# Kernel tuning notes

Hardware: AMD Instinct MI355X
Metric: run time of the kernel (lower is better)

## Reference

```python
import jax, jax.numpy as jnp
import numpy as np

HID = 5120       # hidden_size
H = 32           # num_heads (TP shard)
Q_RANK = 1536    # q_lora_rank
KV_RANK = 512    # kv_lora_rank
D_NOPE = 128     # qk_nope_head_dim
D_ROPE = 64      # qk_rope_head_dim
DV = 128         # v_head_dim
Q_HEAD = D_NOPE + D_ROPE
T = 2048
EPS = 1e-6
ROPE_BASE = 10000.0
SCALE = Q_HEAD ** -0.5
NEG = jnp.finfo(jnp.float32).min


def rmsnorm(x, w):
    return x * jax.lax.rsqrt(jnp.mean(x * x, axis=-1, keepdims=True) + EPS) * w


def rope(x, pos):
    # half-split (GPT-NeoX style) rotary; the torch module permutes weights in
    # _update_pe so that interleaved RoPE becomes exactly this half-split form.
    half = x.shape[-1] // 2
    inv = 1.0 / (ROPE_BASE ** (jnp.arange(half, dtype=jnp.float32) / half))
    ang = pos.astype(jnp.float32)[:, None] * inv          # [T, half]
    cos, sin = jnp.cos(ang), jnp.sin(ang)
    if x.ndim == 3:                                       # [T, H, D]
        cos, sin = cos[:, None, :], sin[:, None, :]
    x1, x2 = jnp.split(x, 2, axis=-1)
    return jnp.concatenate([x1 * cos - x2 * sin, x2 * cos + x1 * sin], axis=-1)


def setup_inputs() -> dict:
    key = jax.random.key(0)
    ks = jax.random.split(key, 10)
    s = 0.02
    return {
        'hidden_states': jax.random.normal(ks[0], (1, T, HID), jnp.float32),
        'position_ids': jnp.arange(T, dtype=jnp.int64),
        'w_q_a': jax.random.normal(ks[1], (Q_RANK, HID), jnp.float32) * s,
        'q_a_ln_w': jnp.ones((Q_RANK,), jnp.float32),
        'w_q_b': jax.random.normal(ks[2], (H * Q_HEAD, Q_RANK), jnp.float32) * s,
        'w_kv_a': jax.random.normal(ks[3], (KV_RANK + D_ROPE, HID), jnp.float32) * s,
        'kv_a_ln_w': jnp.ones((KV_RANK,), jnp.float32),
        'w_kc': jax.random.normal(ks[4], (H, D_NOPE, KV_RANK), jnp.float32) * s,
        'w_vc': jax.random.normal(ks[5], (H, KV_RANK, DV), jnp.float32) * s,
        'w_o': jax.random.normal(ks[6], (HID, H * DV), jnp.float32) * s,
    }


def reference(hidden_states, position_ids, w_q_a, q_a_ln_w, w_q_b, w_kv_a,
              kv_a_ln_w, w_kc, w_vc, w_o):
    h = hidden_states[0]                                   # [T, HID]
    t = h.shape[0]
    # q low-rank path: q_a_proj -> rmsnorm -> q_b_proj
    q = rmsnorm(h @ w_q_a.T, q_a_ln_w) @ w_q_b.T           # [T, H*Q_HEAD]
    q = q.reshape(t, H, Q_HEAD)
    q_nope, q_pe = q[..., :D_NOPE], q[..., D_NOPE:]
    # absorb kv_b (w_kc): project q into the latent kv space
    q_lat = jnp.einsum('thn,hnk->thk', q_nope, w_kc)       # [T, H, KV_RANK]
    # kv low-rank path (MQA-style shared latent)
    ckv_full = h @ w_kv_a.T                                # [T, KV_RANK+D_ROPE]
    ckv = rmsnorm(ckv_full[:, :KV_RANK], kv_a_ln_w)        # [T, KV_RANK]
    k_pe = rope(ckv_full[:, KV_RANK:], position_ids)       # [T, D_ROPE]
    q_pe = rope(q_pe, position_ids)                        # [T, H, D_ROPE]
    # full query/key in latent+pe space; key/value shared across heads
    qf = jnp.concatenate([q_lat, q_pe], axis=-1)           # [T, H, KV_RANK+D_ROPE]
    kf = jnp.concatenate([ckv, k_pe], axis=-1)             # [T, KV_RANK+D_ROPE]
    scores = jnp.einsum('thd,sd->hts', qf, kf) * SCALE     # [H, T, T]
    causal = jnp.tril(jnp.ones((t, t), dtype=bool))
    scores = jnp.where(causal[None], scores, NEG)
    p = jax.nn.softmax(scores, axis=-1)
    o = jnp.einsum('hts,sk->thk', p, ckv)                  # [T, H, KV_RANK]
    o = jnp.einsum('thk,hkv->thv', o, w_vc)                # [T, H, DV]
    out = o.reshape(t, H * DV) @ w_o.T                     # [T, HID]
    return out[None]
```

## Files before the change

### kernel.cpp

```cpp
#include <hip/hip_runtime.h>
#include <hip/hip_bf16.h>
#include <type_traits>

typedef __attribute__((ext_vector_type(8))) short short8;
typedef __attribute__((ext_vector_type(4))) float f32x4;
using bf16 = __hip_bfloat16;

#define T_SEQ 2048
#define NH 32
#define SCALE_F 0.07216878364870323f

__device__ inline unsigned short f2bf(float f) {
    unsigned u = __builtin_bit_cast(unsigned, f);
    return (unsigned short)((u + 0x7fffu + ((u >> 16) & 1u)) >> 16);
}

__device__ inline void gload_lds16(const void* g, void* l) {
    __builtin_amdgcn_global_load_lds(
        (const __attribute__((address_space(1))) unsigned*)g,
        (__attribute__((address_space(3))) unsigned*)l, 16, 0, 0);
}

__device__ inline void cvt8(const float* in, bf16* out, long v, float scale) {
    f32x4 a = *(const f32x4*)(in + v * 8), b = *(const f32x4*)(in + v * 8 + 4);
    short8 r;
    r[0] = (short)f2bf(a[0] * scale); r[1] = (short)f2bf(a[1] * scale);
    r[2] = (short)f2bf(a[2] * scale); r[3] = (short)f2bf(a[3] * scale);
    r[4] = (short)f2bf(b[0] * scale); r[5] = (short)f2bf(b[1] * scale);
    r[6] = (short)f2bf(b[2] * scale); r[7] = (short)f2bf(b[3] * scale);
    *(short8*)(out + v * 8) = r;
}

template <typename TC>
__global__ __launch_bounds__(512, 2) void gemm8p_kernel(
    const bf16* __restrict__ A, const bf16* __restrict__ B, TC* __restrict__ C,
    int K, int lda, int ldb, int ldc)
{
    extern __shared__ char Lds[];
    const int bm = blockIdx.y * 256, bn = blockIdx.x * 256;
    const int tid = threadIdx.x, lane = tid & 63, w = tid >> 6;
    const int l15 = lane & 15, lg = lane >> 4;
    const int wmr = (w >> 2) * 64;
    const int wnc = (w & 3) * 32;
    const int lrh = lane >> 3;
    const int scolb = ((lane & 7) * 16) ^ ((lane >> 3) << 4);
    const int rdswz = (l15 & 7) << 4;
    const bf16* Ab = A + (long)bm * lda;
    const bf16* Bb = B + (long)bn * ldb;
    const int nt = K >> 6;

    auto stage_half = [&](int tt, int isB, int h) {
        const int buf = tt & 1;
        const int k0 = (tt >= nt ? tt - nt : tt) << 6;
        const bf16* Base = isB ? Bb : Ab;
        const int ld = isB ? ldb : lda;
        const char* g = (const char*)Base
            + ((long)(h * 128 + w * 8 + lrh) * ld + k0) * 2 + scolb;
        char* l = Lds + buf * 65536 + isB * 32768 + h * 16384 + w * 1024;
        gload_lds16(g, l);
        gload_lds16(g + (long)128 * ld, l + 8192);
    };

    f32x4 acc[4][4][2] = {};
    stage_half(0, 0, 0); stage_half(0, 1, 1); stage_half(0, 0, 1);
    stage_half(0, 1, 0); stage_half(1, 0, 0); stage_half(1, 1, 1);
    asm volatile("s_waitcnt vmcnt(4)" ::: "memory");
    __builtin_amdgcn_s_barrier();

    for (int t = 0; t < nt; ++t) {
        const char* Bufp = Lds + (t & 1) * 65536;
        short8 aF[4][2], bF[2][2];
        #define ARD(mh, fi, ks) \
            (*(const short8*)(Bufp + (mh) * 16384 + (wmr + (fi) * 16 + l15) * 128 \
                              + (((ks) * 64 + lg * 16) ^ rdswz)))
        #define BRD(nh, nj, ks) \
            (*(const short8*)(Bufp + 32768 + (nh) * 16384 + (wnc + (nj) * 16 + l15) * 128 \
                              + (((ks) * 64 + lg * 16) ^ rdswz)))
        #define MFMA16(q) \
            __builtin_amdgcn_s_setprio(1); \
            _Pragma("unroll") for (int ks = 0; ks < 2; ++ks) \
            _Pragma("unroll") for (int fi = 0; fi < 4; ++fi) \
            _Pragma("unroll") for (int nj = 0; nj < 2; ++nj) \
                acc[q][fi][nj] = __builtin_amdgcn_mfma_f32_16x16x32_bf16( \
                    aF[fi][ks], bF[nj][ks], acc[q][fi][nj], 0, 0, 0); \
            __builtin_amdgcn_s_setprio(0);

        #pragma unroll
        for (int fi = 0; fi < 4; ++fi) { aF[fi][0] = ARD(0, fi, 0); aF[fi][1] = ARD(0, fi, 1); }
        #pragma unroll
        for (int nj = 0; nj < 2; ++nj) { bF[nj][0] = BRD(0, nj, 0); bF[nj][1] = BRD(0, nj, 1); }
        stage_half(t + 1, 0, 1);
        asm volatile("s_waitcnt lgkmcnt(8)" ::: "memory");
        __builtin_amdgcn_s_barrier();
        asm volatile("s_waitcnt lgkmcnt(0)" ::: "memory");
        __builtin_amdgcn_sched_barrier(0);
        MFMA16(0)
        __builtin_amdgcn_s_barrier();
        #pragma unroll
        for (int nj = 0; nj < 2; ++nj) { bF[nj][0] = BRD(1, nj, 0); bF[nj][1] = BRD(1, nj, 1); }
        stage_half(t + 1, 1, 0);
        __builtin_amdgcn_s_barrier();
        asm volatile("s_waitcnt lgkmcnt(0)" ::: "memory");
        __builtin_amdgcn_sched_barrier(0);
        MFMA16(1)
        __builtin_amdgcn_s_barrier();
        #pragma unroll
        for (int fi = 0; fi < 4; ++fi) { aF[fi][0] = ARD(1, fi, 0); aF[fi][1] = ARD(1, fi, 1); }
        stage_half(t + 2, 0, 0);
        __builtin_amdgcn_s_barrier();
        asm volatile("s_waitcnt lgkmcnt(0)" ::: "memory");
        __builtin_amdgcn_sched_barrier(0);
        MFMA16(2)
        __builtin_amdgcn_s_barrier();
        #pragma unroll
        for (int nj = 0; nj < 2; ++nj) { bF[nj][0] = BRD(0, nj, 0); bF[nj][1] = BRD(0, nj, 1); }
        stage_half(t + 2, 1, 1);
        __builtin_amdgcn_s_barrier();
        asm volatile("s_waitcnt lgkmcnt(0)" ::: "memory");
        __builtin_amdgcn_sched_barrier(0);
        MFMA16(3)
        asm volatile("s_waitcnt vmcnt(4)" ::: "memory");
        __builtin_amdgcn_s_barrier();
        #undef ARD
        #undef BRD
        #undef MFMA16
    }
    asm volatile("s_waitcnt vmcnt(0)" ::: "memory");
    const int QMH[4] = {0, 0, 1, 1}, QNH[4] = {0, 1, 1, 0};
    #pragma unroll
    for (int q = 0; q < 4; ++q)
        #pragma unroll
        for (int fi = 0; fi < 4; ++fi)
            #pragma unroll
            for (int nj = 0; nj < 2; ++nj)
                #pragma unroll
                for (int i = 0; i < 4; ++i) {
                    const int row = bm + QMH[q] * 128 + wmr + fi * 16 + lg * 4 + i;
                    const int col = bn + QNH[q] * 128 + wnc + nj * 16 + l15;
                    if constexpr (std::is_same<TC, float>::value)
                        C[(long)row * ldc + col] = acc[q][fi][nj][i];
                    else
                        ((unsigned short*)C)[(long)row * ldc + col] = f2bf(acc[q][fi][nj][i]);
                }
}

template <typename TC>
__global__ __launch_bounds__(256, 2) void gemmhw_kernel(
    const bf16* __restrict__ A, const bf16* __restrict__ B, TC* __restrict__ C,
    int K, int lda, int ldb, int ldc,
    long aStride, long bStride, long cStride)
{
    const int z = blockIdx.z;
    A += (long)z * aStride; B += (long)z * bStride; C += (long)z * cStride;
    const int bm = blockIdx.y * 256, bn = blockIdx.x * 128;
    __shared__ __align__(16) short As[2][256 * 32];
    __shared__ __align__(16) short Bs[2][128 * 32];
    const int tid = threadIdx.x, lane = tid & 63, w = tid >> 6;
    const int l15 = lane & 15, lg = lane >> 4;
    const int wm = w >> 1, wn = w & 1;
    const int sx = (lane & 7) ^ (lane >> 3);
    const int lrh = lane >> 3;
    const int srp = sx >> 2;
    const int scol = (sx & 3) * 8;
    const bf16* Ab = A + (long)bm * lda;
    const bf16* Bb = B + (long)bn * ldb;

    auto stage = [&](int buf, int k0) {
        #pragma unroll
        for (int jj = 0; jj < 4; ++jj) {
            const int j = w * 4 + jj;
            const int srow = 2 * (j * 8 + lrh) + srp;
            gload_lds16(Ab + (long)srow * lda + k0 + scol, &As[buf][j * 512]);
        }
        #pragma unroll
        for (int jj = 0; jj < 2; ++jj) {
            const int j = w * 2 + jj;
            const int srow = 2 * (j * 8 + lrh) + srp;
            gload_lds16(Bb + (long)srow * ldb + k0 + scol, &Bs[buf][j * 512]);
        }
    };

    const int rslot = ((((l15 & 1) << 2) | lg) ^ (l15 >> 1)) << 4;
    const int lrow_lo = l15 >> 1;
    f32x4 acc[8][4] = {};
    const int nt = K >> 5;
    stage(0, 0);
    for (int t = 0; t < nt; ++t) {
        if (t + 1 < nt) {
            stage((t + 1) & 1, (t + 1) << 5);
            asm volatile("s_waitcnt vmcnt(6)" ::: "memory");
        } else {
            asm volatile("s_waitcnt vmcnt(0)" ::: "memory");
        }
        __builtin_amdgcn_s_barrier();
        __builtin_amdgcn_sched_barrier(0);
        const char* Ap = (const char*)&As[t & 1][0];
        const char* Bp = (const char*)&Bs[t & 1][0];
        short8 af[8], bf[4];
        #pragma unroll
        for (int fi = 0; fi < 8; ++fi)
            af[fi] = *(const short8*)(Ap + (wm * 64 + fi * 8 + lrow_lo) * 128 + rslot);
        #pragma unroll
        for (int nj = 0; nj < 4; ++nj)
            bf[nj] = *(const short8*)(Bp + (wn * 32 + nj * 8 + lrow_lo) * 128 + rslot);
        #pragma unroll
        for (int fi = 0; fi < 8; ++fi)
            #pragma unroll
            for (int nj = 0; nj < 4; ++nj)
                acc[fi][nj] = __builtin_amdgcn_mfma_f32_16x16x32_bf16(
                    af[fi], bf[nj], acc[fi][nj], 0, 0, 0);
        asm volatile("s_waitcnt lgkmcnt(0)" ::: "memory");
        __builtin_amdgcn_sched_barrier(0);
        __builtin_amdgcn_s_barrier();
        __builtin_amdgcn_sched_barrier(0);
    }
    #pragma unroll
    for (int fi = 0; fi < 8; ++fi)
        #pragma unroll
        for (int nj = 0; nj < 4; ++nj)
            #pragma unroll
            for (int i = 0; i < 4; ++i) {
                const int row = bm + wm * 128 + fi * 16 + lg * 4 + i;
                const int col = bn + wn * 64 + nj * 16 + l15;
                if constexpr (std::is_same<TC, float>::value)
                    C[(long)row * ldc + col] = acc[fi][nj][i];
                else
                    ((unsigned short*)C)[(long)row * ldc + col] = f2bf(acc[fi][nj][i]);
            }
}

#define GW_NXT 17
#define GW_EXX 8
template <typename TC>
__global__ __launch_bounds__(512, 4) void gemm8w_kernel(
    const bf16* __restrict__ A, const bf16* __restrict__ B, TC* __restrict__ C,
    int K, int lda, int ldb, int ldc,
    const float* __restrict__ cv1in, bf16* __restrict__ cv1out, long n1v, float s1,
    const float* __restrict__ cv2in, bf16* __restrict__ cv2out, long n2v)
{
    const int tid = threadIdx.x;
    if (blockIdx.x >= GW_NXT) {
        const int cb = (blockIdx.x - GW_NXT) * gridDim.y + blockIdx.y;
        const long stride = (long)GW_EXX * gridDim.y * 512;
        for (long v = (long)cb * 512 + tid; v < n1v + n2v; v += stride) {
            if (v < n1v) cvt8(cv1in, cv1out, v, s1);
            else         cvt8(cv2in, cv2out, v - n1v, 1.f);
        }
        return;
    }
    const int bm = blockIdx.y * 128, bn = blockIdx.x * 128;
    __shared__ __align__(16) short As[2][128 * 64];
    __shared__ __align__(16) short Bs[2][128 * 64];
    const int lane = tid & 63, w = tid >> 6;
    const int l15 = lane & 15, lg = lane >> 4;
    const int wm = w >> 1, wn = w & 1;
    const int c0 = w * 2, c1 = w * 2 + 1;
    const int srow0 = c0 * 8 + (lane >> 3), srow1 = c1 * 8 + (lane >> 3);
    const int scol = ((lane & 7) * 16) ^ ((lane >> 3) << 4);
    const bf16* Ab = A + (long)bm * lda;
    const bf16* Bb = B + (long)bn * ldb;

    auto stage = [&](int buf, int k0) {
        const char* ag = (const char*)(Ab + k0);
        const char* bg = (const char*)(Bb + k0);
        gload_lds16(ag + (long)srow0 * (lda * 2) + scol, &As[buf][c0 * 512]);
        gload_lds16(ag + (long)srow1 * (lda * 2) + scol, &As[buf][c1 * 512]);
        gload_lds16(bg + (long)srow0 * (ldb * 2) + scol, &Bs[buf][c0 * 512]);
        gload_lds16(bg + (long)srow1 * (ldb * 2) + scol, &Bs[buf][c1 * 512]);
    };

    const int swz = (l15 & 7) << 4;
    f32x4 acc[2][4] = {};
    const int nt = K >> 6;
    stage(0, 0);
    for (int t = 0; t < nt; ++t) {
        if (t + 1 < nt) {
            stage((t + 1) & 1, (t + 1) << 6);
            asm volatile("s_waitcnt vmcnt(4)" ::: "memory");
        } else {
            asm volatile("s_waitcnt vmcnt(0)" ::: "memory");
        }
        __builtin_amdgcn_s_barrier();
        __builtin_amdgcn_sched_barrier(0);
        const char* Ap = (const char*)&As[t & 1][0];
        const char* Bp = (const char*)&Bs[t & 1][0];
        short8 af[2][2], bfv[4][2];
        #pragma unroll
        for (int fi = 0; fi < 2; ++fi)
            #pragma unroll
            for (int ks = 0; ks < 2; ++ks)
                af[fi][ks] = *(const short8*)(Ap + (wm * 32 + fi * 16 + l15) * 128
                                              + ((ks * 64 + lg * 16) ^ swz));
        #pragma unroll
        for (int nj = 0; nj < 4; ++nj)
            #pragma unroll
            for (int ks = 0; ks < 2; ++ks)
                bfv[nj][ks] = *(const short8*)(Bp + (wn * 64 + nj * 16 + l15) * 128
                                               + ((ks * 64 + lg * 16) ^ swz));
        #pragma unroll
        for (int ks = 0; ks < 2; ++ks)
            #pragma unroll
            for (int fi = 0; fi < 2; ++fi)
                #pragma unroll
                for (int nj = 0; nj < 4; ++nj)
                    acc[fi][nj] = __builtin_amdgcn_mfma_f32_16x16x32_bf16(
                        af[fi][ks], bfv[nj][ks], acc[fi][nj], 0, 0, 0);
        asm volatile("s_waitcnt lgkmcnt(0)" ::: "memory");
        __builtin_amdgcn_sched_barrier(0);
        __builtin_amdgcn_s_barrier();
        __builtin_amdgcn_sched_barrier(0);
    }
    #pragma unroll
    for (int fi = 0; fi < 2; ++fi)
        #pragma unroll
        for (int nj = 0; nj < 4; ++nj)
            #pragma unroll
            for (int i = 0; i < 4; ++i) {
                const int row = bm + wm * 32 + fi * 16 + lg * 4 + i;
                const int col = bn + wn * 64 + nj * 16 + l15;
                if constexpr (std::is_same<TC, float>::value)
                    C[(long)row * ldc + col] = acc[fi][nj][i];
                else
                    ((unsigned short*)C)[(long)row * ldc + col] = f2bf(acc[fi][nj][i]);
            }
}

__global__ __launch_bounds__(256) void cvt_kernel(
    const float* __restrict__ in, bf16* __restrict__ out, long n, float scale)
{
    const long i = (long)blockIdx.x * 256 + threadIdx.x;
    if (i * 8 >= n) return;
    cvt8(in, out, i, scale);
}

__global__ __launch_bounds__(256) void tconv_kernel(
    const float* __restrict__ in, bf16* __restrict__ out)
{
    const int h = blockIdx.z, k0 = blockIdx.x * 32, d0 = blockIdx.y * 32;
    __shared__ float t[32][33];
    const int r = threadIdx.x >> 5, c = threadIdx.x & 31;
    const float* ip = in + ((long)h * 512 + k0) * 128 + d0;
    #pragma unroll
    for (int it = 0; it < 4; ++it)
        t[r + 8 * it][c] = ip[(long)(r + 8 * it) * 128 + c];
    __syncthreads();
    bf16* op = out + ((long)h * 128 + d0) * 512 + k0;
    #pragma unroll
    for (int it = 0; it < 4; ++it)
        op[(long)(r + 8 * it) * 512 + c] = __float2bfloat16(t[c][r + 8 * it]);
}

__global__ __launch_bounds__(256) void rmsnorm2_kernel(
    bf16* __restrict__ x1, const float* __restrict__ w1, int C1,
    bf16* __restrict__ x2, const float* __restrict__ w2, int C2, int ld)
{
    bf16* row;
    const float* w;
    int C;
    if (blockIdx.x < 2048) { row = x1 + (long)blockIdx.x * ld; w = w1; C = C1; }
    else { row = x2 + (long)(blockIdx.x - 2048) * ld; w = w2; C = C2; }
    float ss = 0.f;
    for (int i = threadIdx.x; i < C; i += 256) {
        float v = __bfloat162float(row[i]);
        ss += v * v;
    }
    #pragma unroll
    for (int m = 1; m < 64; m <<= 1) ss += __shfl_xor(ss, m, 64);
    __shared__ float red[4];
    if ((threadIdx.x & 63) == 0) red[threadIdx.x >> 6] = ss;
    __syncthreads();
    ss = red[0] + red[1] + red[2] + red[3];
    float scale = rsqrtf(ss / (float)C + 1e-6f);
    for (int i = threadIdx.x; i < C; i += 256) {
        float v = __bfloat162float(row[i]);
        row[i] = __float2bfloat16(v * scale * w[i]);
    }
}

__global__ __launch_bounds__(256) void ropeq_kernel(bf16* __restrict__ q)
{
    const int t = blockIdx.x;
    #pragma unroll
    for (int it = 0; it < 4; ++it) {
        const int pair = threadIdx.x + 256 * it;
        const int h = pair >> 5, i = pair & 31;
        bf16* base = q + ((long)t * NH + h) * 192;
        float x1 = __bfloat162float(base[128 + i]);
        float x2 = __bfloat162float(base[160 + i]);
        float inv = powf(10000.f, -(float)i / 32.f);
        float ang = (float)t * inv, s, c;
        sincosf(ang, &s, &c);
        base[128 + i] = __float2bfloat16(x1 * c - x2 * s);
        base[160 + i] = __float2bfloat16(x2 * c + x1 * s);
    }
}

__global__ __launch_bounds__(1024) void ropek_kernel(
    const bf16* __restrict__ ckv, bf16* __restrict__ kf, int ld)
{
    const int t = blockIdx.x;
    const int h = threadIdx.x >> 5, i = threadIdx.x & 31;
    float x1 = __bfloat162float(ckv[(long)t * ld + 512 + i]);
    float x2 = __bfloat162float(ckv[(long)t * ld + 544 + i]);
    float inv = powf(10000.f, -(float)i / 32.f);
    float ang = (float)t * inv, s, c;
    sincosf(ang, &s, &c);
    bf16* kb = kf + ((long)h * T_SEQ + t) * 192;
    kb[128 + i] = __float2bfloat16(x1 * c - x2 * s);
    kb[160 + i] = __float2bfloat16(x2 * c + x1 * s);
}

__global__ __launch_bounds__(256, 2) void attn_kernel(
    const bf16* __restrict__ Q,
    const bf16* __restrict__ Kf,
    const bf16* __restrict__ Vt,
    bf16* __restrict__ O,
    const float* __restrict__ WOin, bf16* __restrict__ WOout)
{
    if (blockIdx.x >= 512) {
        const long base = ((long)blockIdx.x - 512) * 2048 + threadIdx.x;
        #pragma unroll
        for (int it = 0; it < 8; ++it)
            cvt8(WOin, WOout, base + (long)it * 256, 1.f);
        return;
    }
    const int lin = blockIdx.x;
    const int h = (lin & 7) + 8 * ((lin >> 3) & 3);
    const int qraw = lin >> 5;
    const int qblk = (qraw < 8) ? (2 * qraw) : (31 - 2 * qraw);
    const int q0 = qblk * 128;
    const int tid = threadIdx.x, lane = tid & 63, w = tid >> 6;
    const int l15 = lane & 15, lg = lane >> 4;
    const int qw = q0 + w * 32;
    __shared__ __align__(16) short Ks[2][64 * 192];
    __shared__ __align__(16) short Vs[2][128 * 64];

    int ksoff[6];
    #pragma unroll
    for (int j = 0; j < 6; ++j) {
        int o = (w * 6 + j) * 1024 + lane * 16;
        int row = o / 384, col = o % 384;
        ksoff[j] = row * 384 + (col ^ ((row & 7) << 4));
    }
    const int vrow8 = lane >> 3;
    const int vscol = ((lane & 7) * 16) ^ (vrow8 << 4);

    short8 qf[2][6];
    #pragma unroll
    for (int qi = 0; qi < 2; ++qi) {
        const bf16* qp = Q + (long)(qw + qi * 16 + l15) * (NH * 192) + (long)h * 192;
        #pragma unroll
        for (int c = 0; c < 6; ++c) qf[qi][c] = *(const short8*)(qp + c * 32 + lg * 8);
    }

    f32x4 oacc[2][8] = {};
    float mst[2] = {-INFINITY, -INFINITY};
    float lst[2] = {0.f, 0.f};

    const char* kbase0 = (const char*)Kf + (long)h * T_SEQ * 384;
    const char* vbase0 = (const char*)Vt + (long)h * 128 * (T_SEQ * 2);
    const int swz = (l15 & 7) << 4;
    const int nt = (q0 + 128) >> 6;

    auto stage = [&](int t) {
        char* KsB = (char*)&Ks[t & 1][0];
        char* VsB = (char*)&Vs[t & 1][0];
        const char* kb = kbase0 + (long)(t * 64) * 384;
        #pragma unroll
        for (int j = 0; j < 6; ++j)
            gload_lds16(kb + ksoff[j], KsB + (w * 6 + j) * 1024);
        const char* vb = vbase0 + (long)(t * 64) * 2 + vscol;
        #pragma unroll
        for (int j = 0; j < 4; ++j) {
            const int c = w * 4 + j;
            gload_lds16(vb + (long)(c * 8 + vrow8) * (T_SEQ * 2), VsB + c * 1024);
        }
    };

    stage(0);
    for (int t = 0; t < nt; ++t) {
        const int s0 = t * 64;
        if (t + 1 < nt) {
            stage(t + 1);
            asm volatile("s_waitcnt vmcnt(10)" ::: "memory");
        } else {
            asm volatile("s_waitcnt vmcnt(0)" ::: "memory");
        }
        __builtin_amdgcn_s_barrier();
        __builtin_amdgcn_sched_barrier(0);
        if (s0 <= qw + 31) {
            const char* KsB = (const char*)&Ks[t & 1][0];
            const char* VsB = (const char*)&Vs[t & 1][0];
            f32x4 st[2][4] = {};
            __builtin_amdgcn_s_setprio(1);
            #pragma unroll
            for (int cb = 0; cb < 4; ++cb) {
                const int krow = cb * 16 + l15;
                #pragma unroll
                for (int c = 0; c < 6; ++c) {
                    short8 kfr = *(const short8*)(KsB + krow * 384
                                                  + ((c * 64 + lg * 16) ^ swz));
                    st[0][cb] = __builtin_amdgcn_mfma_f32_16x16x32_bf16(kfr, qf[0][c], st[0][cb], 0, 0, 0);
                    st[1][cb] = __builtin_amdgcn_mfma_f32_16x16x32_bf16(kfr, qf[1][c], st[1][cb], 0, 0, 0);
                }
            }
            __builtin_amdgcn_s_setprio(0);
            float pmaxv[2];
            #pragma unroll
            for (int qi = 0; qi < 2; ++qi) {
                const int qg = qw + qi * 16 + l15;
                float pmax = -INFINITY;
                #pragma unroll
                for (int cb = 0; cb < 4; ++cb)
                    #pragma unroll
                    for (int i = 0; i < 4; ++i) {
                        const int kv = s0 + cb * 16 + lg * 4 + i;
                        float v = (kv <= qg) ? st[qi][cb][i] : -INFINITY;
                        st[qi][cb][i] = v;
                        pmax = fmaxf(pmax, v);
                    }
                pmax = fmaxf(pmax, __shfl_xor(pmax, 16, 64));
                pmax = fmaxf(pmax, __shfl_xor(pmax, 32, 64));
                pmaxv[qi] = pmax;
            }
            const bool full = !__all((pmaxv[0] - mst[0] <= 8.f) &&
                                     (pmaxv[1] - mst[1] <= 8.f));
            short8 pb[2][2];
            #pragma unroll
            for (int qi = 0; qi < 2; ++qi) {
                float mm;
                if (full) {
                    const float newm = fmaxf(mst[qi], pmaxv[qi]);
                    mm = (newm == -INFINITY) ? 0.f : newm;
                    const float alpha = __expf(mst[qi] - mm);
                    lst[qi] *= alpha;
                    mst[qi] = newm;
                    #pragma unroll
                    for (int mb = 0; mb < 8; ++mb) oacc[qi][mb] *= alpha;
                } else {
                    mm = mst[qi];
                }
                float ps = 0.f;
                #pragma unroll
                for (int cb = 0; cb < 4; ++cb)
                    #pragma unroll
                    for (int i = 0; i < 4; ++i) {
                        const float e = __expf(st[qi][cb][i] - mm);
                        st[qi][cb][i] = e; ps += e;
                    }
                ps += __shfl_xor(ps, 16, 64);
                ps += __shfl_xor(ps, 32, 64);
                lst[qi] += ps;
                #pragma unroll
                for (int hh = 0; hh < 2; ++hh) {
                    unsigned pk[4];
                    #pragma unroll
                    for (int i = 0; i < 4; ++i)
                        pk[i] = (unsigned)f2bf(st[qi][2 * hh][i])
                              | ((unsigned)f2bf(st[qi][2 * hh + 1][i]) << 16);
                    #pragma unroll
                    for (int j = 0; j < 8; ++j) {
                        const int src = l15 + (((2 * lg + (j >> 2)) & 3) << 4);
                        const unsigned u = (unsigned)__shfl((int)pk[j & 3], src, 64);
                        pb[qi][hh][j] = (short)((lg >> 1) ? (u >> 16) : (u & 0xffffu));
                    }
                }
            }
            __builtin_amdgcn_s_setprio(1);
            #pragma unroll
            for (int mb = 0; mb < 8; ++mb) {
                const int vrow = mb * 16 + l15;
                #pragma unroll
                for (int hh = 0; hh < 2; ++hh) {
                    short8 vfr = *(const short8*)(VsB + vrow * 128
                                                  + ((hh * 64 + lg * 16) ^ swz));
                    oacc[0][mb] = __builtin_amdgcn_mfma_f32_16x16x32_bf16(vfr, pb[0][hh], oacc[0][mb], 0, 0, 0);
                    oacc[1][mb] = __builtin_amdgcn_mfma_f32_16x16x32_bf16(vfr, pb[1][hh], oacc[1][mb], 0, 0, 0);
                }
            }
            __builtin_amdgcn_s_setprio(0);
        }
        __builtin_amdgcn_sched_barrier(0);
        __builtin_amdgcn_s_barrier();
    }
    #pragma unroll
    for (int qi = 0; qi < 2; ++qi) {
        const float inv = 1.f / lst[qi];
        const int qg = qw + qi * 16 + l15;
        #pragma unroll
        for (int mb = 0; mb < 8; ++mb)
            #pragma unroll
            for (int i = 0; i < 4; ++i) {
                const int dv = mb * 16 + lg * 4 + i;
                O[(long)qg * (NH * 128) + h * 128 + dv] = __float2bfloat16(oacc[qi][mb][i] * inv);
            }
    }
}

extern "C" void kernel_launch(void* const* d_in, const int* in_sizes, int n_in,
                              void* d_out, int out_size, void* d_ws, size_t ws_size,
                              hipStream_t stream)
{
    const float* hidden    = (const float*)d_in[0];
    const float* w_q_a     = (const float*)d_in[2];
    const float* q_a_ln_w  = (const float*)d_in[3];
    const float* w_q_b     = (const float*)d_in[4];
    const float* w_kv_a    = (const float*)d_in[5];
    const float* kv_a_ln_w = (const float*)d_in[6];
    const float* w_kc      = (const float*)d_in[7];
    const float* w_vc      = (const float*)d_in[8];
    const float* w_o       = (const float*)d_in[9];
    float* out = (float*)d_out;

    bf16* qckv  = (bf16*)d_ws;
    bf16* qbuf  = qckv  + (long)T_SEQ * 2176;
    bf16* kf    = qbuf  + (long)T_SEQ * 6144;
    bf16* vt    = kf    + (long)NH * T_SEQ * 192;
    bf16* ov    = vt    + (long)NH * 128 * T_SEQ;
    bf16* hb    = ov    + (long)T_SEQ * 4096;
    bf16* wqckv = hb    + (long)T_SEQ * 5120;
    bf16* wqb   = wqckv + (long)2176 * 5120;
    bf16* wkc   = wqb   + (long)6144 * 1536;
    bf16* wvct  = wkc   + (long)NH * 128 * 512;
    bf16* wo    = hb;
    bf16* ckv   = qckv + 1536;

    cvt_kernel<<<dim3(5120), 256, 0, stream>>>(hidden, hb, (long)T_SEQ * 5120, 1.f);
    cvt_kernel<<<dim3(3840), 256, 0, stream>>>(w_q_a, wqckv, (long)1536 * 5120, 1.f);
    cvt_kernel<<<dim3(1440), 256, 0, stream>>>(w_kv_a, wqckv + (long)1536 * 5120,
                                               (long)576 * 5120, 1.f);
    hipMemsetAsync(wqckv + (long)2112 * 5120, 0, (long)64 * 5120 * sizeof(bf16), stream);
    tconv_kernel<<<dim3(16, 4, NH), 256, 0, stream>>>(w_vc, wvct);

    gemm8w_kernel<bf16><<<dim3(GW_NXT + GW_EXX, 16, 1), 512, 0, stream>>>(
        hb, wqckv, qckv, 5120, 5120, 5120, 2176,
        w_q_b, wqb, (long)6144 * 1536 / 8, SCALE_F,
        w_kc, wkc, (long)NH * 128 * 512 / 8);
    rmsnorm2_kernel<<<dim3(4096), 256, 0, stream>>>(
        qckv, q_a_ln_w, 1536, ckv, kv_a_ln_w, 512, 2176);
    gemm8p_kernel<bf16><<<dim3(24, 8), 512, 131072, stream>>>(
        qckv, wqb, qbuf, 1536, 2176, 1536, 6144);
    ropeq_kernel<<<dim3(T_SEQ), 256, 0, stream>>>(qbuf);
    ropek_kernel<<<dim3(T_SEQ), 1024, 0, stream>>>(ckv, kf, 2176);
    gemmhw_kernel<bf16><<<dim3(1, 8, NH), 256, 0, stream>>>(
        ckv, wkc, kf, 512, 2176, 512, 192,
        0, (long)128 * 512, (long)T_SEQ * 192);
    gemm8p_kernel<bf16><<<dim3(8, 16), 512, 131072, stream>>>(
        wvct, ckv, vt, 512, 512, 2176, 2048);
    attn_kernel<<<dim3(1792), 256, 0, stream>>>(qbuf, kf, vt, ov, w_o, wo);
    gemm8p_kernel<float><<<dim3(20, 8), 512, 131072, stream>>>(
        ov, wo, out, 4096, 4096, 4096, 5120);
}
```

Before: 441.7 us.

## Merge conversion launches, single-buffer attention KV staging, switch Vt GEMM kernel

Replaces the three fp32-to-bf16 conversion launches and the memset with one grid-stride kernel that also writes the zero padding. Reverts the attention kernel's double-buffered async K/V prefetch to a single LDS buffer that is loaded and then synchronised each tile. Also computes the transposed V projection with the gemmhw kernel instead of gemm8p. The first change cuts launch overhead and the LDS cut may raise occupancy, but attention loses its overlap of loads with MFMA work.

Result: no change. 440.4 us, median of 2 (-0.3%).

```diff
diff --git a/kernel.cpp b/kernel.cpp
--- a/kernel.cpp
+++ b/kernel.cpp
@@ -325,12 +325,25 @@
             }
 }
 
-__global__ __launch_bounds__(256) void cvt_kernel(
-    const float* __restrict__ in, bf16* __restrict__ out, long n, float scale)
-{
-    const long i = (long)blockIdx.x * 256 + threadIdx.x;
-    if (i * 8 >= n) return;
-    cvt8(in, out, i, scale);
+__global__ __launch_bounds__(256) void cvtall_kernel(
+    const float* __restrict__ hid, bf16* __restrict__ hb,
+    const float* __restrict__ wqa, const float* __restrict__ wkva,
+    bf16* __restrict__ wqckv)
+{
+    const long N0 = (long)T_SEQ * 5120 / 8;
+    const long N1 = N0 + (long)1536 * 5120 / 8;
+    const long N2 = N1 + (long)576 * 5120 / 8;
+    const long N3 = N2 + (long)64 * 5120 / 8;
+    const long stride = (long)gridDim.x * 256;
+    for (long v = (long)blockIdx.x * 256 + threadIdx.x; v < N3; v += stride) {
+        if (v < N0) cvt8(hid, hb, v, 1.f);
+        else if (v < N1) cvt8(wqa, wqckv, v - N0, 1.f);
+        else if (v < N2) cvt8(wkva, wqckv + (long)1536 * 5120, v - N1, 1.f);
+        else {
+            short8 z = {};
+            *(short8*)(wqckv + (long)2112 * 5120 + (v - N2) * 8) = z;
+        }
+    }
 }
 
 __global__ __launch_bounds__(256) void tconv_kernel(
@@ -432,8 +445,8 @@
     const int tid = threadIdx.x, lane = tid & 63, w = tid >> 6;
     const int l15 = lane & 15, lg = lane >> 4;
     const int qw = q0 + w * 32;
-    __shared__ __align__(16) short Ks[2][64 * 192];
-    __shared__ __align__(16) short Vs[2][128 * 64];
+    __shared__ __align__(16) short Ks[64 * 192];
+    __shared__ __align__(16) short Vs[128 * 64];
 
     int ksoff[6];
     #pragma unroll
@@ -460,37 +473,23 @@
     const char* kbase0 = (const char*)Kf + (long)h * T_SEQ * 384;
     const char* vbase0 = (const char*)Vt + (long)h * 128 * (T_SEQ * 2);
     const int swz = (l15 & 7) << 4;
-    const int nt = (q0 + 128) >> 6;
-
-    auto stage = [&](int t) {
-        char* KsB = (char*)&Ks[t & 1][0];
-        char* VsB = (char*)&Vs[t & 1][0];
-        const char* kb = kbase0 + (long)(t * 64) * 384;
-        #pragma unroll
-        for (int j = 0; j < 6; ++j)
-            gload_lds16(kb + ksoff[j], KsB + (w * 6 + j) * 1024);
-        const char* vb = vbase0 + (long)(t * 64) * 2 + vscol;
-        #pragma unroll
-        for (int j = 0; j < 4; ++j) {
-            const int c = w * 4 + j;
-            gload_lds16(vb + (long)(c * 8 + vrow8) * (T_SEQ * 2), VsB + c * 1024);
-        }
-    };
-
-    stage(0);
-    for (int t = 0; t < nt; ++t) {
-        const int s0 = t * 64;
-        if (t + 1 < nt) {
-            stage(t + 1);
-            asm volatile("s_waitcnt vmcnt(10)" ::: "memory");
-        } else {
-            asm volatile("s_waitcnt vmcnt(0)" ::: "memory");
-        }
-        __builtin_amdgcn_s_barrier();
-        __builtin_amdgcn_sched_barrier(0);
+
+    for (int s0 = 0; s0 < q0 + 128; s0 += 64) {
+        {
+            const char* kb = kbase0 + (long)s0 * 384;
+            #pragma unroll
+            for (int j = 0; j < 6; ++j)
+                gload_lds16(kb + ksoff[j], (char*)Ks + (w * 6 + j) * 1024);
+            const char* vb = vbase0 + (long)s0 * 2 + vscol;
+            #pragma unroll
+            for (int j = 0; j < 4; ++j) {
+                const int c = w * 4 + j;
+                gload_lds16(vb + (long)(c * 8 + vrow8) * (T_SEQ * 2),
+                            (char*)Vs + c * 1024);
+            }
+        }
+        __syncthreads();
         if (s0 <= qw + 31) {
-            const char* KsB = (const char*)&Ks[t & 1][0];
-            const char* VsB = (const char*)&Vs[t & 1][0];
             f32x4 st[2][4] = {};
             __builtin_amdgcn_s_setprio(1);
             #pragma unroll
@@ -498,7 +497,7 @@
                 const int krow = cb * 16 + l15;
                 #pragma unroll
                 for (int c = 0; c < 6; ++c) {
-                    short8 kfr = *(const short8*)(KsB + krow * 384
+                    short8 kfr = *(const short8*)((const char*)Ks + krow * 384
                                                   + ((c * 64 + lg * 16) ^ swz));
                     st[0][cb] = __builtin_amdgcn_mfma_f32_16x16x32_bf16(kfr, qf[0][c], st[0][cb], 0, 0, 0);
                     st[1][cb] = __builtin_amdgcn_mfma_f32_16x16x32_bf16(kfr, qf[1][c], st[1][cb], 0, 0, 0);
@@ -572,7 +571,7 @@
                 const int vrow = mb * 16 + l15;
                 #pragma unroll
                 for (int hh = 0; hh < 2; ++hh) {
-                    short8 vfr = *(const short8*)(VsB + vrow * 128
+                    short8 vfr = *(const short8*)((const char*)Vs + vrow * 128
                                                   + ((hh * 64 + lg * 16) ^ swz));
                     oacc[0][mb] = __builtin_amdgcn_mfma_f32_16x16x32_bf16(vfr, pb[0][hh], oacc[0][mb], 0, 0, 0);
                     oacc[1][mb] = __builtin_amdgcn_mfma_f32_16x16x32_bf16(vfr, pb[1][hh], oacc[1][mb], 0, 0, 0);
@@ -580,8 +579,7 @@
             }
             __builtin_amdgcn_s_setprio(0);
         }
-        __builtin_amdgcn_sched_barrier(0);
-        __builtin_amdgcn_s_barrier();
+        __syncthreads();
     }
     #pragma unroll
     for (int qi = 0; qi < 2; ++qi) {
@@ -625,11 +623,7 @@
     bf16* wo    = hb;
     bf16* ckv   = qckv + 1536;
 
-    cvt_kernel<<<dim3(5120), 256, 0, stream>>>(hidden, hb, (long)T_SEQ * 5120, 1.f);
-    cvt_kernel<<<dim3(3840), 256, 0, stream>>>(w_q_a, wqckv, (long)1536 * 5120, 1.f);
-    cvt_kernel<<<dim3(1440), 256, 0, stream>>>(w_kv_a, wqckv + (long)1536 * 5120,
-                                               (long)576 * 5120, 1.f);
-    hipMemsetAsync(wqckv + (long)2112 * 5120, 0, (long)64 * 5120 * sizeof(bf16), stream);
+    cvtall_kernel<<<dim3(2048), 256, 0, stream>>>(hidden, hb, w_q_a, w_kv_a, wqckv);
     tconv_kernel<<<dim3(16, 4, NH), 256, 0, stream>>>(w_vc, wvct);
 
     gemm8w_kernel<bf16><<<dim3(GW_NXT + GW_EXX, 16, 1), 512, 0, stream>>>(
@@ -645,8 +639,8 @@
     gemmhw_kernel<bf16><<<dim3(1, 8, NH), 256, 0, stream>>>(
         ckv, wkc, kf, 512, 2176, 512, 192,
         0, (long)128 * 512, (long)T_SEQ * 192);
-    gemm8p_kernel<bf16><<<dim3(8, 16), 512, 131072, stream>>>(
-        wvct, ckv, vt, 512, 512, 2176, 2048);
+    gemmhw_kernel<bf16><<<dim3(16, 16, 1), 256, 0, stream>>>(
+        wvct, ckv, vt, 512, 512, 2176, 2048, 0, 0, 0);
     attn_kernel<<<dim3(1792), 256, 0, stream>>>(qbuf, kf, vt, ov, w_o, wo);
     gemm8p_kernel<float><<<dim3(20, 8), 512, 131072, stream>>>(
         ov, wo, out, 4096, 4096, 4096, 5120);
```
